# Optimization experiments

Hardware: AMD Instinct MI355X
Metric: run time of the kernel (lower is better)

## Reference

```python
import jax, jax.numpy as jnp
import numpy as np

T, H, I, E, SI, TOP_K = 1024, 2048, 1408, 60, 5632, 4


def setup_inputs() -> dict:
    key = jax.random.key(0)
    ks = jax.random.split(key, 9)
    s = 0.02  # typical init scale for weights
    return {
        "x": jax.random.normal(ks[0], (T, H), jnp.float32),
        "router_w": jax.random.normal(ks[1], (E, H), jnp.float32) * s,
        "w_gate": jax.random.normal(ks[2], (E, I, H), jnp.float32) * s,
        "w_up": jax.random.normal(ks[3], (E, I, H), jnp.float32) * s,
        "w_down": jax.random.normal(ks[4], (E, H, I), jnp.float32) * s,
        "sw_gate": jax.random.normal(ks[5], (SI, H), jnp.float32) * s,
        "sw_up": jax.random.normal(ks[6], (SI, H), jnp.float32) * s,
        "sw_down": jax.random.normal(ks[7], (H, SI), jnp.float32) * s,
        "shared_gate_w": jax.random.normal(ks[8], (1, H), jnp.float32) * s,
        "top_k": TOP_K,
    }


def reference(x, router_w, w_gate, w_up, w_down, sw_gate, sw_up, sw_down, shared_gate_w, top_k):
    Ttok, Hdim = x.shape
    Eexp = router_w.shape[0]
    # --- router: softmax over experts, top-k selection (norm_topk_prob=False) ---
    logits = x @ router_w.T                          # [T,E]
    probs = jax.nn.softmax(logits, axis=-1)
    topk_p, topk_i = jax.lax.top_k(probs, top_k)     # [T,k]
    # dense combine weights: zero for unrouted experts
    combine = jnp.zeros((Ttok, Eexp), x.dtype)
    combine = combine.at[jnp.arange(Ttok)[:, None], topk_i].set(topk_p)  # [T,E]

    # --- routed experts: SwiGLU MLP per expert, weighted accumulate (scan over E) ---
    def expert_step(acc, w):
        wg, wu, wd, c = w                            # [I,H],[I,H],[H,I],[T]
        h = jax.nn.silu(x @ wg.T) * (x @ wu.T)       # [T,I]
        return acc + c[:, None] * (h @ wd.T), None

    moe_out, _ = jax.lax.scan(expert_step, jnp.zeros_like(x),
                              (w_gate, w_up, w_down, combine.T))

    # --- shared expert with sigmoid gate ---
    shared = (jax.nn.silu(x @ sw_gate.T) * (x @ sw_up.T)) @ sw_down.T    # [T,H]
    shared = jax.nn.sigmoid(x @ shared_gate_w.T) * shared                # [T,1]*[T,H]
    return moe_out + shared
```

## Files before the change

### kernel.cpp

```cpp
#include <hip/hip_runtime.h>
#include <hip/hip_bf16.h>


typedef float  f32x4  __attribute__((ext_vector_type(4)));
typedef short  bf16x8 __attribute__((ext_vector_type(8)));
typedef unsigned short u16;
typedef unsigned int   u32;

constexpr int TT = 1024, HD = 2048, ID = 1408, NE = 60, SID = 5632, KTOP = 4;
constexpr int NBR_GU = (ID / 64) * NE;
constexpr int NB_GU  = NBR_GU + (SID / 64) * (TT / 128);
constexpr int NBS_DN = (HD / 64) * (TT / 128);
constexpr int NB_DN  = NBS_DN + (HD / 64) * NE;

#define GLDS(g, l) __builtin_amdgcn_global_load_lds( \
    (const __attribute__((address_space(1))) void*)(g), \
    (__attribute__((address_space(3))) void*)(l), 16, 0, 0)
#define GL4(dst, ptr) asm volatile("global_load_dwordx4 %0, %1, off" : "=&v"(dst) : "v"(ptr))
#define WAITVM(n) do { asm volatile("s_waitcnt vmcnt(" #n ")" ::: "memory"); \
                       __builtin_amdgcn_sched_barrier(0); } while (0)
#define LGKMBAR() do { asm volatile("s_waitcnt lgkmcnt(0)" ::: "memory"); \
    __builtin_amdgcn_s_barrier(); \
    asm volatile("" ::: "memory"); } while (0)

__device__ __forceinline__ u16 f2bf(float f) {
    union { float f; u32 u; } v; v.f = f;
    u32 r = v.u + 0x7FFFu + ((v.u >> 16) & 1u);
    return (u16)(r >> 16);
}
__device__ __forceinline__ u32 cvtpk(float a, float b) {
    u32 r; asm("v_cvt_pk_bf16_f32 %0, %1, %2" : "=v"(r) : "v"(a), "v"(b));
    return r;
}
__device__ __forceinline__ bf16x8 cvt8(f32x4 a, f32x4 b) {
    union { u32 u[4]; bf16x8 v; } rr;
    rr.u[0] = cvtpk(a[0], a[1]); rr.u[1] = cvtpk(a[2], a[3]);
    rr.u[2] = cvtpk(b[0], b[1]); rr.u[3] = cvtpk(b[2], b[3]);
    return rr.v;
}

__global__ void zero_k(int* __restrict__ p) { p[threadIdx.x] = 0; }

__global__ __launch_bounds__(256) void zeroout_k(float* __restrict__ p) {
    ((float4*)p)[blockIdx.x * 256 + threadIdx.x] = make_float4(0.f, 0.f, 0.f, 0.f);
}

__global__ __launch_bounds__(256) void xcvt_k(const float* __restrict__ x, u16* __restrict__ xb)
{
    size_t i = ((size_t)blockIdx.x * 256 + threadIdx.x) * 16;
    const float4* p = (const float4*)(x + i);
    float4 f0 = p[0], f1 = p[1], f2 = p[2], f3 = p[3];
    uint4 o0, o1;
    o0.x = cvtpk(f0.x, f0.y); o0.y = cvtpk(f0.z, f0.w);
    o0.z = cvtpk(f1.x, f1.y); o0.w = cvtpk(f1.z, f1.w);
    o1.x = cvtpk(f2.x, f2.y); o1.y = cvtpk(f2.z, f2.w);
    o1.z = cvtpk(f3.x, f3.y); o1.w = cvtpk(f3.z, f3.w);
    ((uint4*)(xb + i))[0] = o0;
    ((uint4*)(xb + i))[1] = o1;
}

__global__ __launch_bounds__(64) void router_k(
    const float* __restrict__ x, const float* __restrict__ rw,
    const float* __restrict__ sgw,
    float* __restrict__ topk_p, int* __restrict__ topk_i,
    int* __restrict__ cnt, float* __restrict__ sgate)
{
    const int t = blockIdx.x, l = threadIdx.x;
    const float4* xr = ((const float4*)(x + (size_t)t * HD)) + l * 8;
    float4 xa[8];
    #pragma unroll
    for (int i = 0; i < 8; i++) xa[i] = xr[i];

    float le = 0.f;
    for (int e = 0; e < NE; e++) {
        const float4* wr = ((const float4*)(rw + (size_t)e * HD)) + l * 8;
        float a = 0.f;
        #pragma unroll
        for (int i = 0; i < 8; i++) {
            float4 wv = wr[i];
            a += xa[i].x * wv.x + xa[i].y * wv.y + xa[i].z * wv.z + xa[i].w * wv.w;
        }
        #pragma unroll
        for (int s = 32; s; s >>= 1) a += __shfl_xor(a, s);
        if (l == e) le = a;
    }
    {
        const float4* wr = ((const float4*)sgw) + l * 8;
        float a = 0.f;
        #pragma unroll
        for (int i = 0; i < 8; i++) {
            float4 wv = wr[i];
            a += xa[i].x * wv.x + xa[i].y * wv.y + xa[i].z * wv.z + xa[i].w * wv.w;
        }
        #pragma unroll
        for (int s = 32; s; s >>= 1) a += __shfl_xor(a, s);
        if (l == 0) sgate[t] = 1.f / (1.f + __expf(-a));
    }
    float mv = (l < NE) ? le : -3.4e38f;
    #pragma unroll
    for (int s = 32; s; s >>= 1) mv = fmaxf(mv, __shfl_xor(mv, s));
    float p = (l < NE) ? __expf(le - mv) : 0.f;
    float ss = p;
    #pragma unroll
    for (int s = 32; s; s >>= 1) ss += __shfl_xor(ss, s);
    p /= ss;
    float pv = (l < NE) ? p : -1.f;
    int   pi = l;
    float kp = 0.f; int ki = 0;
    for (int k = 0; k < KTOP; k++) {
        float bv = pv; int bi = pi;
        #pragma unroll
        for (int s = 32; s; s >>= 1) {
            float ov = __shfl_xor(bv, s); int oi = __shfl_xor(bi, s);
            if (ov > bv || (ov == bv && oi < bi)) { bv = ov; bi = oi; }
        }
        if (l == k) { kp = bv; ki = bi; }
        if (pi == bi) pv = -1.f;
    }
    if (l < KTOP) {
        topk_p[t * KTOP + l] = kp;
        topk_i[t * KTOP + l] = ki;
        atomicAdd(&cnt[ki], 1);
    }
}

__global__ __launch_bounds__(64) void prefix_k(const int* __restrict__ cnt, int* __restrict__ base)
{
    int l = threadIdx.x;
    if (l < NE) {
        int s = 0;
        for (int j = 0; j < l; j++) s += cnt[j];
        base[l] = s;
    }
}

__global__ __launch_bounds__(256) void scatter_k(
    const float* __restrict__ topk_p, const int* __restrict__ topk_i,
    const int* __restrict__ base, int* __restrict__ fill,
    int* __restrict__ slot_tok, float* __restrict__ slot_wt)
{
    int t = blockIdx.x * blockDim.x + threadIdx.x;
    if (t >= TT) return;
    for (int k = 0; k < KTOP; k++) {
        int e = topk_i[t * KTOP + k];
        int pos = atomicAdd(&fill[e], 1);
        int s = base[e] + pos;
        slot_tok[s] = t;
        slot_wt[s]  = topk_p[t * KTOP + k];
    }
}

__global__ __launch_bounds__(256, 2) void gu_all(
    const u16* __restrict__ Xb,
    const float* __restrict__ w_gate, const float* __restrict__ w_up,
    const float* __restrict__ sw_g, const float* __restrict__ sw_u,
    u16* __restrict__ h, u16* __restrict__ hs,
    const int* __restrict__ slot_tok, const float* __restrict__ slot_wt,
    const int* __restrict__ cnt, const int* __restrict__ basea)
{
    __shared__ u16 Asl[4][128 * 32];
    __shared__ u16 Bgsl[2][64 * 32];
    __shared__ u16 Busl[2][64 * 32];

    const int bid = blockIdx.x;
    const bool grouped = bid < NBR_GU;
    const int tid = threadIdx.x, w = tid >> 6, lane = tid & 63;
    const int lm = lane & 15, lk = lane >> 4;
    const int wm0 = (w >> 1) * 64, wn0 = (w & 1) * 32;

    int e = 0, my = 0, nb;
    const float *Wg, *Wu; u16* Hout; int Nout;
    if (grouped) {
        e = bid / 22; nb = bid % 22;
        Wg = w_gate + (size_t)e * ID * HD; Wu = w_up + (size_t)e * ID * HD;
        Hout = h; Nout = ID;
    } else {
        int sid = bid - NBR_GU; my = sid / 88; nb = sid % 88;
        Wg = sw_g; Wu = sw_u; Hout = hs; Nout = SID;
    }
    const int mcnt  = grouped ? cnt[e] : 128;
    const int mbase = grouped ? basea[e] : 0;

    const int aCh = (((lane & 3) ^ ((lane >> 2) & 3) ^ ((lane >> 4) & 3))) << 3;
    const int brow_s = tid >> 2, bkc = tid & 3;
    const float* pg = Wg + (size_t)(nb * 64 + brow_s) * HD + bkc * 8;
    const float* pu = Wu + (size_t)(nb * 64 + brow_s) * HD + bkc * 8;
    const int bWr = brow_s * 32 + ((bkc ^ ((brow_s >> 1) & 3)) << 3);

    int aOff[4], bOff[2];
    #pragma unroll
    for (int mf = 0; mf < 4; mf++) {
        int r = wm0 + mf * 16 + lm;
        aOff[mf] = r * 32 + ((lk ^ (r & 3) ^ ((r >> 2) & 3)) << 3);
    }
    #pragma unroll
    for (int nf = 0; nf < 2; nf++) {
        int rb = wn0 + nf * 16 + lm;
        bOff[nf] = rb * 32 + ((lk ^ ((rb >> 1) & 3)) << 3);
    }
    const int segA0 = (w * 32) * 32, segA1 = (w * 32 + 16) * 32;
    const int nk = HD >> 5;

    for (int mt = 0; grouped ? (mt * 128 < mcnt) : (mt == 0); ++mt) {
        const u16* aSrc0; const u16* aSrc1;
        {
            int m0 = w * 32 + (lane >> 2), m1 = m0 + 16;
            int r0, r1;
            if (grouped) {
                int s0 = mbase + mt * 128 + m0, s1 = mbase + mt * 128 + m1;
                r0 = (mt * 128 + m0 < mcnt) ? slot_tok[s0] : slot_tok[mbase];
                r1 = (mt * 128 + m1 < mcnt) ? slot_tok[s1] : slot_tok[mbase];
            } else { r0 = my * 128 + m0; r1 = my * 128 + m1; }
            aSrc0 = Xb + (size_t)r0 * HD + aCh;
            aSrc1 = Xb + (size_t)r1 * HD + aCh;
        }

        f32x4 accG[4][2], accU[4][2];
        #pragma unroll
        for (int mf = 0; mf < 4; mf++)
            #pragma unroll
            for (int nf = 0; nf < 2; nf++) {
                accG[mf][nf] = f32x4{0.f, 0.f, 0.f, 0.f};
                accU[mf][nf] = f32x4{0.f, 0.f, 0.f, 0.f};
            }

        f32x4 ga0, ga1, ua0, ua1;
        f32x4 gb0, gb1, ub0, ub1;

#define ISSUE(G0_, G1_, U0_, U1_, AB, KT) do {                                \
        GL4(G0_, pg + (KT)); GL4(G1_, pg + (KT) + 4);                         \
        GL4(U0_, pu + (KT)); GL4(U1_, pu + (KT) + 4);                         \
        GLDS(aSrc0 + (KT), &Asl[AB][segA0]);                                  \
        GLDS(aSrc1 + (KT), &Asl[AB][segA1]);                                  \
    } while (0)

#define WRITEB(G0_, G1_, U0_, U1_, BB) do {                                   \
        *(bf16x8*)&Bgsl[BB][bWr] = cvt8(G0_, G1_);                            \
        *(bf16x8*)&Busl[BB][bWr] = cvt8(U0_, U1_);                            \
    } while (0)

#define COMPSTEP(AB, BB) do {                                                 \
        bf16x8 af[4], bg[2], bu_[2];                                          \
        _Pragma("unroll")                                                     \
        for (int mf = 0; mf < 4; mf++) af[mf] = *(const bf16x8*)&Asl[AB][aOff[mf]]; \
        _Pragma("unroll")                                                     \
        for (int nf = 0; nf < 2; nf++) {                                      \
            bg[nf]  = *(const bf16x8*)&Bgsl[BB][bOff[nf]];                    \
            bu_[nf] = *(const bf16x8*)&Busl[BB][bOff[nf]];                    \
        }                                                                     \
        _Pragma("unroll")                                                     \
        for (int mf = 0; mf < 4; mf++)                                        \
            _Pragma("unroll")                                                 \
            for (int nf = 0; nf < 2; nf++) {                                  \
                accG[mf][nf] = __builtin_amdgcn_mfma_f32_16x16x32_bf16(af[mf], bg[nf],  accG[mf][nf], 0, 0, 0); \
                accU[mf][nf] = __builtin_amdgcn_mfma_f32_16x16x32_bf16(af[mf], bu_[nf], accU[mf][nf], 0, 0, 0); \
            }                                                                 \
    } while (0)

        ISSUE(ga0, ga1, ua0, ua1, 0, 0);
        ISSUE(gb0, gb1, ub0, ub1, 1, 32);
        WAITVM(6);
        WRITEB(ga0, ga1, ua0, ua1, 0);
        LGKMBAR();

        for (int t = 0; t < nk; t += 4) {
            if (t + 2 < nk) { ISSUE(ga0, ga1, ua0, ua1, 2, (t + 2) << 5); COMPSTEP(0, 0); WAITVM(6); }
            else            { COMPSTEP(0, 0); WAITVM(0); }
            if (t + 1 < nk) WRITEB(gb0, gb1, ub0, ub1, 1);
            LGKMBAR();
            if (t + 3 < nk) { ISSUE(gb0, gb1, ub0, ub1, 3, (t + 3) << 5); COMPSTEP(1, 1); WAITVM(6); }
            else            { COMPSTEP(1, 1); WAITVM(0); }
            if (t + 2 < nk) WRITEB(ga0, ga1, ua0, ua1, 0);
            LGKMBAR();
            if (t + 4 < nk) { ISSUE(ga0, ga1, ua0, ua1, 0, (t + 4) << 5); COMPSTEP(2, 0); WAITVM(6); }
            else            { COMPSTEP(2, 0); WAITVM(0); }
            if (t + 3 < nk) WRITEB(gb0, gb1, ub0, ub1, 1);
            LGKMBAR();
            if (t + 5 < nk) { ISSUE(gb0, gb1, ub0, ub1, 1, (t + 5) << 5); COMPSTEP(3, 1); WAITVM(6); }
            else            { COMPSTEP(3, 1); WAITVM(0); }
            if (t + 4 < nk) WRITEB(ga0, ga1, ua0, ua1, 0);
            LGKMBAR();
        }
#undef ISSUE
#undef WRITEB
#undef COMPSTEP

        #pragma unroll
        for (int mf = 0; mf < 4; mf++)
            #pragma unroll
            for (int j = 0; j < 4; j++) {
                int m = wm0 + mf * 16 + lk * 4 + j;
                bool valid = grouped ? (mt * 128 + m < mcnt) : true;
                if (valid) {
                    size_t row; float wt;
                    if (grouped) {
                        size_t sl = (size_t)(mbase + mt * 128 + m);
                        row = sl; wt = slot_wt[sl];
                    } else { row = (size_t)(my * 128 + m); wt = 1.f; }
                    #pragma unroll
                    for (int nf = 0; nf < 2; nf++) {
                        int col = nb * 64 + wn0 + nf * 16 + lm;
                        float g = accG[mf][nf][j], u = accU[mf][nf][j];
                        float hv = g / (1.f + __expf(-g)) * u * wt;
                        Hout[row * (size_t)Nout + col] = f2bf(hv);
                    }
                }
            }
    }
}

__global__ __launch_bounds__(256, 3) void down_all(
    const u16* __restrict__ h, const u16* __restrict__ hs,
    const float* __restrict__ w_down, const float* __restrict__ sw_d,
    float* __restrict__ outF,
    const int* __restrict__ slot_tok, const float* __restrict__ sgate,
    const int* __restrict__ cnt, const int* __restrict__ basea)
{
    __shared__ u16 Asl[4][128 * 32];
    __shared__ u16 Bsl[2][64 * 32];

    const int bid = blockIdx.x;
    const bool shared_m = bid < NBS_DN;
    const int tid = threadIdx.x, w = tid >> 6, lane = tid & 63;
    const int lm = lane & 15, lk = lane >> 4;
    const int wm0 = (w >> 1) * 64, wn0 = (w & 1) * 32;

    int e = 0, my = 0, nb, K;
    const u16* Ap; const float* Wp;
    if (shared_m) {
        my = bid / 32; nb = bid % 32; K = SID; Ap = hs; Wp = sw_d;
    } else {
        int rid = bid - NBS_DN; e = rid / 32; nb = rid % 32; K = ID;
        Ap = h; Wp = w_down + (size_t)e * HD * ID;
    }
    const int mcnt  = shared_m ? 128 : cnt[e];
    const int mbase = shared_m ? 0 : basea[e];

    const int aCh = (((lane & 3) ^ ((lane >> 2) & 3) ^ ((lane >> 4) & 3))) << 3;
    const int brow_s = tid >> 2, bkc = tid & 3;
    const float* pb = Wp + (size_t)(nb * 64 + brow_s) * K + bkc * 8;
    const int bWr = brow_s * 32 + ((bkc ^ ((brow_s >> 1) & 3)) << 3);

    int aOff[4], bOff[2];
    #pragma unroll
    for (int mf = 0; mf < 4; mf++) {
        int r = wm0 + mf * 16 + lm;
        aOff[mf] = r * 32 + ((lk ^ (r & 3) ^ ((r >> 2) & 3)) << 3);
    }
    #pragma unroll
    for (int nf = 0; nf < 2; nf++) {
        int rb = wn0 + nf * 16 + lm;
        bOff[nf] = rb * 32 + ((lk ^ ((rb >> 1) & 3)) << 3);
    }
    const int segA0 = (w * 32) * 32, segA1 = (w * 32 + 16) * 32;
    const int nk = K >> 5;

    for (int mt = 0; shared_m ? (mt == 0) : (mt * 128 < mcnt); ++mt) {
        const u16* aSrc0; const u16* aSrc1;
        {
            int m0 = w * 32 + (lane >> 2), m1 = m0 + 16;
            size_t r0, r1;
            if (shared_m) { r0 = (size_t)(my * 128 + m0); r1 = (size_t)(my * 128 + m1); }
            else { r0 = (size_t)(mbase + mt * 128 + m0); r1 = (size_t)(mbase + mt * 128 + m1); }
            aSrc0 = Ap + r0 * K + aCh;
            aSrc1 = Ap + r1 * K + aCh;
        }

        f32x4 acc[4][2];
        #pragma unroll
        for (int mf = 0; mf < 4; mf++)
            #pragma unroll
            for (int nf = 0; nf < 2; nf++) acc[mf][nf] = f32x4{0.f, 0.f, 0.f, 0.f};

        f32x4 ba0, ba1;
        f32x4 bb0, bb1;

#define ISSUE(B0_, B1_, AB, KT) do {                                          \
        GL4(B0_, pb + (KT)); GL4(B1_, pb + (KT) + 4);                         \
        GLDS(aSrc0 + (KT), &Asl[AB][segA0]);                                  \
        GLDS(aSrc1 + (KT), &Asl[AB][segA1]);                                  \
    } while (0)

#define WRITEB(B0_, B1_, BB) do {                                             \
        *(bf16x8*)&Bsl[BB][bWr] = cvt8(B0_, B1_);                             \
    } while (0)

#define COMPSTEP(AB, BB) do {                                                 \
        bf16x8 af[4], bf_[2];                                                 \
        _Pragma("unroll")                                                     \
        for (int mf = 0; mf < 4; mf++) af[mf] = *(const bf16x8*)&Asl[AB][aOff[mf]]; \
        _Pragma("unroll")                                                     \
        for (int nf = 0; nf < 2; nf++) bf_[nf] = *(const bf16x8*)&Bsl[BB][bOff[nf]]; \
        _Pragma("unroll")                                                     \
        for (int mf = 0; mf < 4; mf++)                                        \
            _Pragma("unroll")                                                 \
            for (int nf = 0; nf < 2; nf++)                                    \
                acc[mf][nf] = __builtin_amdgcn_mfma_f32_16x16x32_bf16(af[mf], bf_[nf], acc[mf][nf], 0, 0, 0); \
    } while (0)

        ISSUE(ba0, ba1, 0, 0);
        ISSUE(bb0, bb1, 1, 32);
        WAITVM(4);
        WRITEB(ba0, ba1, 0);
        LGKMBAR();

        for (int t = 0; t < nk; t += 4) {
            if (t + 2 < nk) { ISSUE(ba0, ba1, 2, (t + 2) << 5); COMPSTEP(0, 0); WAITVM(4); }
            else            { COMPSTEP(0, 0); WAITVM(0); }
            if (t + 1 < nk) WRITEB(bb0, bb1, 1);
            LGKMBAR();
            if (t + 3 < nk) { ISSUE(bb0, bb1, 3, (t + 3) << 5); COMPSTEP(1, 1); WAITVM(4); }
            else            { COMPSTEP(1, 1); WAITVM(0); }
            if (t + 2 < nk) WRITEB(ba0, ba1, 0);
            LGKMBAR();
            if (t + 4 < nk) { ISSUE(ba0, ba1, 0, (t + 4) << 5); COMPSTEP(2, 0); WAITVM(4); }
            else            { COMPSTEP(2, 0); WAITVM(0); }
            if (t + 3 < nk) WRITEB(bb0, bb1, 1);
            LGKMBAR();
            if (t + 5 < nk) { ISSUE(bb0, bb1, 1, (t + 5) << 5); COMPSTEP(3, 1); WAITVM(4); }
            else            { COMPSTEP(3, 1); WAITVM(0); }
            if (t + 4 < nk) WRITEB(ba0, ba1, 0);
            LGKMBAR();
        }
#undef ISSUE
#undef WRITEB
#undef COMPSTEP

        #pragma unroll
        for (int mf = 0; mf < 4; mf++)
            #pragma unroll
            for (int j = 0; j < 4; j++) {
                int m = wm0 + mf * 16 + lk * 4 + j;
                if (mt * 128 + m < mcnt) {
                    int tok; float scale;
                    if (shared_m) { tok = my * 128 + m; scale = sgate[tok]; }
                    else          { tok = slot_tok[mbase + mt * 128 + m]; scale = 1.f; }
                    #pragma unroll
                    for (int nf = 0; nf < 2; nf++) {
                        int col = nb * 64 + wn0 + nf * 16 + lm;
                        atomicAdd(&outF[(size_t)tok * HD + col], scale * acc[mf][nf][j]);
                    }
                }
            }
    }
}

extern "C" void kernel_launch(void* const* d_in, const int* in_sizes, int n_in,
                              void* d_out, int out_size, void* d_ws, size_t ws_size,
                              hipStream_t stream)
{
    const float* x      = (const float*)d_in[0];
    const float* rw     = (const float*)d_in[1];
    const float* w_gate = (const float*)d_in[2];
    const float* w_up   = (const float*)d_in[3];
    const float* w_down = (const float*)d_in[4];
    const float* sw_g   = (const float*)d_in[5];
    const float* sw_u   = (const float*)d_in[6];
    const float* sw_d   = (const float*)d_in[7];
    const float* sgw    = (const float*)d_in[8];
    float* out = (float*)d_out;

    char* ws = (char*)d_ws;
    int*   cnt      = (int*)(ws + 0);
    int*   fill     = (int*)(ws + 256);
    int*   basea    = (int*)(ws + 512);
    float* sgate    = (float*)(ws + 768);
    float* topk_p   = (float*)(ws + 5120);
    int*   topk_i   = (int*)(ws + 21504);
    int*   slot_tok = (int*)(ws + 37888);
    float* slot_wt  = (float*)(ws + 54272);
    u16*   xb = (u16*)(ws + 71680);
    u16*   h  = xb + (size_t)TT * HD;
    u16*   hs = h + (size_t)(4096 + 128) * ID;

    zero_k<<<1, 128, 0, stream>>>(cnt);
    zeroout_k<<<TT * HD / 1024, 256, 0, stream>>>(out);
    xcvt_k<<<512, 256, 0, stream>>>(x, xb);
    router_k<<<TT, 64, 0, stream>>>(x, rw, sgw, topk_p, topk_i, cnt, sgate);
    prefix_k<<<1, 64, 0, stream>>>(cnt, basea);
    scatter_k<<<4, 256, 0, stream>>>(topk_p, topk_i, basea, fill, slot_tok, slot_wt);

    gu_all<<<NB_GU, 256, 0, stream>>>(
        xb, w_gate, w_up, sw_g, sw_u, h, hs,
        slot_tok, slot_wt, cnt, basea);

    down_all<<<NB_DN, 256, 0, stream>>>(
        h, hs, w_down, sw_d, out,
        slot_tok, sgate, cnt, basea);
}
```

Baseline: 781.8 us.

## Widen gate/up tile to 128 columns with 512-thread blocks

```diff
diff --git a/kernel.cpp b/kernel.cpp
--- a/kernel.cpp
+++ b/kernel.cpp
@@ -8,8 +8,8 @@
 typedef unsigned int   u32;
 
 constexpr int TT = 1024, HD = 2048, ID = 1408, NE = 60, SID = 5632, KTOP = 4;
-constexpr int NBR_GU = (ID / 64) * NE;
-constexpr int NB_GU  = NBR_GU + (SID / 64) * (TT / 128);
+constexpr int NBR_GU = (ID / 128) * NE;
+constexpr int NB_GU  = NBR_GU + (SID / 128) * (TT / 128);
 constexpr int NBS_DN = (HD / 64) * (TT / 128);
 constexpr int NB_DN  = NBS_DN + (HD / 64) * NE;
 
@@ -150,7 +150,7 @@
     }
 }
 
-__global__ __launch_bounds__(256, 2) void gu_all(
+__global__ __launch_bounds__(512, 2) void gu_all(
     const u16* __restrict__ Xb,
     const float* __restrict__ w_gate, const float* __restrict__ w_up,
     const float* __restrict__ sw_g, const float* __restrict__ sw_u,
@@ -159,33 +159,35 @@
     const int* __restrict__ cnt, const int* __restrict__ basea)
 {
     __shared__ u16 Asl[4][128 * 32];
-    __shared__ u16 Bgsl[2][64 * 32];
-    __shared__ u16 Busl[2][64 * 32];
+    __shared__ u16 Bgsl[2][128 * 32];
+    __shared__ u16 Busl[2][128 * 32];
 
     const int bid = blockIdx.x;
     const bool grouped = bid < NBR_GU;
     const int tid = threadIdx.x, w = tid >> 6, lane = tid & 63;
     const int lm = lane & 15, lk = lane >> 4;
-    const int wm0 = (w >> 1) * 64, wn0 = (w & 1) * 32;
+    const int wm0 = (w >> 2) * 64, wn0 = (w & 3) * 32;
 
     int e = 0, my = 0, nb;
     const float *Wg, *Wu; u16* Hout; int Nout;
     if (grouped) {
-        e = bid / 22; nb = bid % 22;
+        e = bid / 11; nb = bid % 11;
         Wg = w_gate + (size_t)e * ID * HD; Wu = w_up + (size_t)e * ID * HD;
         Hout = h; Nout = ID;
     } else {
-        int sid = bid - NBR_GU; my = sid / 88; nb = sid % 88;
+        int sid = bid - NBR_GU; my = sid / 44; nb = sid % 44;
         Wg = sw_g; Wu = sw_u; Hout = hs; Nout = SID;
     }
     const int mcnt  = grouped ? cnt[e] : 128;
     const int mbase = grouped ? basea[e] : 0;
 
-    const int aCh = (((lane & 3) ^ ((lane >> 2) & 3) ^ ((lane >> 4) & 3))) << 3;
-    const int brow_s = tid >> 2, bkc = tid & 3;
-    const float* pg = Wg + (size_t)(nb * 64 + brow_s) * HD + bkc * 8;
-    const float* pu = Wu + (size_t)(nb * 64 + brow_s) * HD + bkc * 8;
-    const int bWr = brow_s * 32 + ((bkc ^ ((brow_s >> 1) & 3)) << 3);
+    const int ars = tid >> 2;
+    const int aCh = (((tid & 3) ^ (ars & 3) ^ ((ars >> 2) & 3))) << 3;
+    const int segA = (w * 16) * 32;
+    const int brt = tid >> 2, bkc = tid & 3;
+    const float* pg = Wg + (size_t)(nb * 128 + brt) * HD + bkc * 8;
+    const float* pu = Wu + (size_t)(nb * 128 + brt) * HD + bkc * 8;
+    const int bWr = brt * 32 + ((bkc ^ ((brt >> 1) & 3)) << 3);
 
     int aOff[4], bOff[2];
     #pragma unroll
@@ -198,21 +200,17 @@
         int rb = wn0 + nf * 16 + lm;
         bOff[nf] = rb * 32 + ((lk ^ ((rb >> 1) & 3)) << 3);
     }
-    const int segA0 = (w * 32) * 32, segA1 = (w * 32 + 16) * 32;
     const int nk = HD >> 5;
 
     for (int mt = 0; grouped ? (mt * 128 < mcnt) : (mt == 0); ++mt) {
-        const u16* aSrc0; const u16* aSrc1;
+        const u16* aSrc;
         {
-            int m0 = w * 32 + (lane >> 2), m1 = m0 + 16;
-            int r0, r1;
+            int row;
             if (grouped) {
-                int s0 = mbase + mt * 128 + m0, s1 = mbase + mt * 128 + m1;
-                r0 = (mt * 128 + m0 < mcnt) ? slot_tok[s0] : slot_tok[mbase];
-                r1 = (mt * 128 + m1 < mcnt) ? slot_tok[s1] : slot_tok[mbase];
-            } else { r0 = my * 128 + m0; r1 = my * 128 + m1; }
-            aSrc0 = Xb + (size_t)r0 * HD + aCh;
-            aSrc1 = Xb + (size_t)r1 * HD + aCh;
+                int sl = mbase + mt * 128 + ars;
+                row = (mt * 128 + ars < mcnt) ? slot_tok[sl] : slot_tok[mbase];
+            } else row = my * 128 + ars;
+            aSrc = Xb + (size_t)row * HD + aCh;
         }
 
         f32x4 accG[4][2], accU[4][2];
@@ -230,8 +228,7 @@
 #define ISSUE(G0_, G1_, U0_, U1_, AB, KT) do {                                \
         GL4(G0_, pg + (KT)); GL4(G1_, pg + (KT) + 4);                         \
         GL4(U0_, pu + (KT)); GL4(U1_, pu + (KT) + 4);                         \
-        GLDS(aSrc0 + (KT), &Asl[AB][segA0]);                                  \
-        GLDS(aSrc1 + (KT), &Asl[AB][segA1]);                                  \
+        GLDS(aSrc + (KT), &Asl[AB][segA]);                                    \
     } while (0)
 
 #define WRITEB(G0_, G1_, U0_, U1_, BB) do {                                   \
@@ -259,24 +256,24 @@
 
         ISSUE(ga0, ga1, ua0, ua1, 0, 0);
         ISSUE(gb0, gb1, ub0, ub1, 1, 32);
-        WAITVM(6);
+        WAITVM(5);
         WRITEB(ga0, ga1, ua0, ua1, 0);
         LGKMBAR();
 
         for (int t = 0; t < nk; t += 4) {
-            if (t + 2 < nk) { ISSUE(ga0, ga1, ua0, ua1, 2, (t + 2) << 5); COMPSTEP(0, 0); WAITVM(6); }
+            if (t + 2 < nk) { ISSUE(ga0, ga1, ua0, ua1, 2, (t + 2) << 5); COMPSTEP(0, 0); WAITVM(5); }
             else            { COMPSTEP(0, 0); WAITVM(0); }
             if (t + 1 < nk) WRITEB(gb0, gb1, ub0, ub1, 1);
             LGKMBAR();
-            if (t + 3 < nk) { ISSUE(gb0, gb1, ub0, ub1, 3, (t + 3) << 5); COMPSTEP(1, 1); WAITVM(6); }
+            if (t + 3 < nk) { ISSUE(gb0, gb1, ub0, ub1, 3, (t + 3) << 5); COMPSTEP(1, 1); WAITVM(5); }
             else            { COMPSTEP(1, 1); WAITVM(0); }
             if (t + 2 < nk) WRITEB(ga0, ga1, ua0, ua1, 0);
             LGKMBAR();
-            if (t + 4 < nk) { ISSUE(ga0, ga1, ua0, ua1, 0, (t + 4) << 5); COMPSTEP(2, 0); WAITVM(6); }
+            if (t + 4 < nk) { ISSUE(ga0, ga1, ua0, ua1, 0, (t + 4) << 5); COMPSTEP(2, 0); WAITVM(5); }
             else            { COMPSTEP(2, 0); WAITVM(0); }
             if (t + 3 < nk) WRITEB(gb0, gb1, ub0, ub1, 1);
             LGKMBAR();
-            if (t + 5 < nk) { ISSUE(gb0, gb1, ub0, ub1, 1, (t + 5) << 5); COMPSTEP(3, 1); WAITVM(6); }
+            if (t + 5 < nk) { ISSUE(gb0, gb1, ub0, ub1, 1, (t + 5) << 5); COMPSTEP(3, 1); WAITVM(5); }
             else            { COMPSTEP(3, 1); WAITVM(0); }
             if (t + 4 < nk) WRITEB(ga0, ga1, ua0, ua1, 0);
             LGKMBAR();
@@ -299,7 +296,7 @@
                     } else { row = (size_t)(my * 128 + m); wt = 1.f; }
                     #pragma unroll
                     for (int nf = 0; nf < 2; nf++) {
-                        int col = nb * 64 + wn0 + nf * 16 + lm;
+                        int col = nb * 128 + wn0 + nf * 16 + lm;
                         float g = accG[mf][nf][j], u = accU[mf][nf][j];
                         float hv = g / (1.f + __expf(-g)) * u * wt;
                         Hout[row * (size_t)Nout + col] = f2bf(hv);
@@ -480,7 +477,7 @@
     prefix_k<<<1, 64, 0, stream>>>(cnt, basea);
     scatter_k<<<4, 256, 0, stream>>>(topk_p, topk_i, basea, fill, slot_tok, slot_wt);
 
-    gu_all<<<NB_GU, 256, 0, stream>>>(
+    gu_all<<<NB_GU, 512, 0, stream>>>(
         xb, w_gate, w_up, sw_g, sw_u, h, hs,
         slot_tok, slot_wt, cnt, basea);
 
```

Result: slower. 819.5 us (+4.8%).
